# Kernel tuning notes

Measured on AMD Instinct MI355X. Metric: run time of the kernel, lower is better.

Reference implementation:

```python
import jax, jax.numpy as jnp
import numpy as np

N_CLUSTERS = 8
N_DIMS = 4
N_POINTS = 2_000_000


def setup_inputs() -> dict:
    key = jax.random.key(0)
    k1, k2, k3, k4 = jax.random.split(key, 4)
    return {
        "X": jax.random.normal(k1, (N_POINTS, N_DIMS), dtype=jnp.float32),
        "means": jax.random.normal(k2, (N_CLUSTERS, N_DIMS), dtype=jnp.float32),
        "chols": jax.random.normal(k3, (N_CLUSTERS, N_DIMS, N_DIMS), dtype=jnp.float32),
        "weights": jax.random.normal(k4, (N_CLUSTERS,), dtype=jnp.float32),
        "it": 0,
    }


def reference(X, means, chols, weights, it):
    N, D = X.shape
    K = means.shape[0]
    # sigmas[k] = tril(L_k) @ tril(L_k)^T + I  (cholesky_comp)
    L = jnp.tril(chols)                                   # [K,D,D]
    sigmas = L @ jnp.swapaxes(L, -1, -2) + jnp.eye(D, dtype=X.dtype)
    S_inv = jnp.linalg.inv(sigmas)                        # [K,D,D]
    dets = jnp.linalg.det(sigmas)                         # [K]
    two_pi_D = (2.0 * jnp.pi) ** D
    # per-cluster Gaussian densities over all points: dens[k,n]
    diff = X[None, :, :] - means[:, None, :]              # [K,N,D]
    mahal = jnp.einsum('knd,kde,kne->kn', diff, S_inv, diff)  # [K,N]
    dens = jnp.exp(-0.5 * mahal) / jnp.sqrt(two_pi_D * dets)[:, None]
    # pairwise softmax weights over all K^2 (i,j) products w_i*w_j
    wij = weights[:, None] * weights[None, :]             # [K,K]
    W = jax.nn.softmax(wij.reshape(-1)).reshape(K, K)
    # squared-mixture normaliser: z = sum_ij W_ij * N(mu_i; mu_j, S_i+S_j)
    Ssum = sigmas[:, None] + sigmas[None, :]              # [K,K,D,D]
    det_sum = jnp.linalg.det(Ssum)                        # [K,K]
    mdiff = means[:, None, :] - means[None, :, :]         # [K,K,D]
    md = jnp.einsum('ijd,ijde,ije->ij', mdiff, jnp.linalg.inv(Ssum), mdiff)
    norm_term = jnp.exp(-0.5 * md) / jnp.sqrt(two_pi_D * det_sum)
    z = jnp.sum(W * norm_term)
    # numerator: sum_ij W_ij dens_i dens_j  (factored to avoid [K^2,N])
    num = jnp.einsum('in,jn,ij->n', dens, dens, W)        # [N]
    pdf = num / z
    # forward: -(logsumexp over points of log pdf) / N
    out = -(jax.scipy.special.logsumexp(jnp.log(pdf)) / N)
    return out
```

## Files before the change

kernel.cpp:

```cpp
#include <hip/hip_runtime.h>
#include <math.h>


#define KC 8

struct WsLayout {
  double P[36];
  double W[64];
  double logz;
  double pad_;
  float a2[8][10];
  float bb[8][4];
  float cc[8];
};

__device__ inline void chol4(const double S[4][4], double G[4][4]) {
  #pragma unroll
  for (int i = 0; i < 4; ++i) {
    #pragma unroll
    for (int j = 0; j < 4; ++j) {
      if (j > i) { G[i][j] = 0.0; continue; }
      double s = S[i][j];
      #pragma unroll
      for (int m = 0; m < 4; ++m) if (m < j) s -= G[i][m] * G[j][m];
      if (i == j) G[i][j] = sqrt(s);
      else        G[i][j] = s / G[j][j];
    }
  }
}

__global__ void prep_kernel(const float* __restrict__ means,
                            const float* __restrict__ chols,
                            const float* __restrict__ weights,
                            WsLayout* ws) {
  __shared__ double sig[8][4][4];
  const double LOG2E = 1.4426950408889634074;
  const double LN2PI = 1.8378770664093454836;
  const int t = threadIdx.x;

  if (t < 8) {
    const int k = t;
    double L[4][4], S[4][4];
    #pragma unroll
    for (int i = 0; i < 4; ++i)
      #pragma unroll
      for (int j = 0; j < 4; ++j)
        L[i][j] = (j <= i) ? (double)chols[k * 16 + i * 4 + j] : 0.0;
    #pragma unroll
    for (int i = 0; i < 4; ++i)
      #pragma unroll
      for (int j = 0; j < 4; ++j) {
        double s = (i == j) ? 1.0 : 0.0;
        #pragma unroll
        for (int m = 0; m < 4; ++m) s += L[i][m] * L[j][m];
        S[i][j] = s;
        sig[k][i][j] = s;
      }
    double G[4][4];
    chol4(S, G);
    const double logdet =
        2.0 * (log(G[0][0]) + log(G[1][1]) + log(G[2][2]) + log(G[3][3]));
    double Gi[4][4];
    #pragma unroll
    for (int j = 0; j < 4; ++j) {
      #pragma unroll
      for (int i = 0; i < 4; ++i) {
        if (i < j) { Gi[i][j] = 0.0; continue; }
        double s = (i == j) ? 1.0 : 0.0;
        #pragma unroll
        for (int m = 0; m < 4; ++m)
          if (m >= j && m < i) s -= G[i][m] * Gi[m][j];
        Gi[i][j] = s / G[i][i];
      }
    }
    double A[4][4];
    #pragma unroll
    for (int i = 0; i < 4; ++i)
      #pragma unroll
      for (int j = 0; j < 4; ++j) {
        double s = 0.0;
        #pragma unroll
        for (int m = 0; m < 4; ++m) s += Gi[m][i] * Gi[m][j];
        A[i][j] = s;
      }
    double mu[4];
    #pragma unroll
    for (int i = 0; i < 4; ++i) mu[i] = (double)means[k * 4 + i];
    double bmu[4];
    #pragma unroll
    for (int i = 0; i < 4; ++i) {
      double s = 0.0;
      #pragma unroll
      for (int j = 0; j < 4; ++j) s += A[i][j] * mu[j];
      bmu[i] = s;
    }
    double muAmu = 0.0;
    #pragma unroll
    for (int i = 0; i < 4; ++i) muAmu += mu[i] * bmu[i];
    const double logcoef = -0.5 * (4.0 * LN2PI + logdet);
    int tt = 0;
    #pragma unroll
    for (int i = 0; i < 4; ++i)
      #pragma unroll
      for (int j = i; j < 4; ++j, ++tt)
        ws->a2[k][tt] =
            (float)(-0.5 * LOG2E * A[i][j] * ((i == j) ? 1.0 : 2.0));
    #pragma unroll
    for (int i = 0; i < 4; ++i) ws->bb[k][i] = (float)(LOG2E * bmu[i]);
    ws->cc[k] = (float)(LOG2E * (logcoef - 0.5 * muAmu));
  }
  __syncthreads();

  const int i = t >> 3, j = t & 7;
  const double wij = (double)weights[i] * (double)weights[j];
  double m = wij;
  #pragma unroll
  for (int o = 32; o > 0; o >>= 1) {
    double x = __shfl_xor(m, o, 64);
    m = fmax(m, x);
  }
  const double e = exp(wij - m);
  double ssum = e;
  #pragma unroll
  for (int o = 32; o > 0; o >>= 1) ssum += __shfl_xor(ssum, o, 64);
  const double Wij = e / ssum;

  double SS[4][4];
  #pragma unroll
  for (int a = 0; a < 4; ++a)
    #pragma unroll
    for (int b = 0; b < 4; ++b) SS[a][b] = sig[i][a][b] + sig[j][a][b];
  double G2[4][4];
  chol4(SS, G2);
  const double logdetS =
      2.0 * (log(G2[0][0]) + log(G2[1][1]) + log(G2[2][2]) + log(G2[3][3]));
  double bvec[4], y[4];
  #pragma unroll
  for (int a = 0; a < 4; ++a)
    bvec[a] = (double)means[i * 4 + a] - (double)means[j * 4 + a];
  #pragma unroll
  for (int a = 0; a < 4; ++a) {
    double s = bvec[a];
    #pragma unroll
    for (int mm = 0; mm < 4; ++mm) if (mm < a) s -= G2[a][mm] * y[mm];
    y[a] = s / G2[a][a];
  }
  const double md = y[0]*y[0] + y[1]*y[1] + y[2]*y[2] + y[3]*y[3];
  double zterm = Wij * exp(-0.5 * md - 0.5 * (4.0 * LN2PI + logdetS));
  #pragma unroll
  for (int o = 32; o > 0; o >>= 1) zterm += __shfl_xor(zterm, o, 64);
  if (t == 0) ws->logz = log(zterm);
  ws->W[t] = Wij;
  if (t < 36) ws->P[t] = 0.0;
}

__global__ __launch_bounds__(256) void point_kernel(
    const float4* __restrict__ X, const float* __restrict__ par,
    double* __restrict__ accg, int n) {
  float a2[8][10], bb[8][4], cc[8];
  #pragma unroll
  for (int k = 0; k < 8; ++k) {
    #pragma unroll
    for (int u = 0; u < 10; ++u) a2[k][u] = par[k * 10 + u];
    #pragma unroll
    for (int u = 0; u < 4; ++u) bb[k][u] = par[80 + k * 4 + u];
    cc[k] = par[112 + k];
  }
  float acc[36];
  #pragma unroll
  for (int u = 0; u < 36; ++u) acc[u] = 0.0f;

  const int idx = blockIdx.x * blockDim.x + threadIdx.x;
  const int stride = gridDim.x * blockDim.x;
  for (int i = idx; i < n; i += stride) {
    const float4 v = X[i];
    const float p[10] = {v.x * v.x, v.x * v.y, v.x * v.z, v.x * v.w,
                         v.y * v.y, v.y * v.z, v.y * v.w,
                         v.z * v.z, v.z * v.w, v.w * v.w};
    float d[8];
    #pragma unroll
    for (int k = 0; k < 8; ++k) {
      float a = cc[k];
      #pragma unroll
      for (int u = 0; u < 10; ++u) a = fmaf(a2[k][u], p[u], a);
      a = fmaf(bb[k][0], v.x, a);
      a = fmaf(bb[k][1], v.y, a);
      a = fmaf(bb[k][2], v.z, a);
      a = fmaf(bb[k][3], v.w, a);
      d[k] = __builtin_amdgcn_exp2f(a);
    }
    int u = 0;
    #pragma unroll
    for (int a_ = 0; a_ < 8; ++a_)
      #pragma unroll
      for (int b_ = a_; b_ < 8; ++b_, ++u)
        acc[u] = fmaf(d[a_], d[b_], acc[u]);
  }

  const int lane = threadIdx.x & 63;
  const int wid = threadIdx.x >> 6;
  __shared__ float lred[4][36];
  #pragma unroll
  for (int u = 0; u < 36; ++u) {
    float vv = acc[u];
    #pragma unroll
    for (int o = 32; o > 0; o >>= 1) vv += __shfl_xor(vv, o, 64);
    if (lane == 0) lred[wid][u] = vv;
  }
  __syncthreads();
  if (threadIdx.x < 36) {
    const double s = (double)lred[0][threadIdx.x] + (double)lred[1][threadIdx.x] +
                     (double)lred[2][threadIdx.x] + (double)lred[3][threadIdx.x];
    unsafeAtomicAdd(&accg[threadIdx.x], s);
  }
}

__global__ void final_kernel(const WsLayout* __restrict__ ws,
                             float* __restrict__ out, int n) {
  double tot = 0.0;
  int u = 0;
  #pragma unroll
  for (int i = 0; i < 8; ++i)
    #pragma unroll
    for (int j = i; j < 8; ++j, ++u) {
      const double w = ws->W[i * 8 + j] * ((i == j) ? 1.0 : 2.0);
      tot += w * ws->P[u];
    }
  out[0] = (float)(-(log(tot) - ws->logz) / (double)n);
}

extern "C" void kernel_launch(void* const* d_in, const int* in_sizes, int n_in,
                              void* d_out, int out_size, void* d_ws, size_t ws_size,
                              hipStream_t stream) {
  const float* X       = (const float*)d_in[0];
  const float* means   = (const float*)d_in[1];
  const float* chols   = (const float*)d_in[2];
  const float* weights = (const float*)d_in[3];
  const int npoints = in_sizes[0] / 4;

  WsLayout* ws = (WsLayout*)d_ws;
  prep_kernel<<<1, 64, 0, stream>>>(means, chols, weights, ws);
  point_kernel<<<1024, 256, 0, stream>>>((const float4*)X, &ws->a2[0][0],
                                         ws->P, npoints);
  final_kernel<<<1, 1, 0, stream>>>(ws, (float*)d_out, npoints);
}
```

Before: 117.2 us.

## Spread atomics over 32 slots, batch 4 loads per thread, double grid

Global atomic accumulation now goes to 32 separate copies of each of the 36 sums, indexed by block, which are reduced in a 64-thread final kernel. The point loop loads 4 points per iteration to raise memory-level parallelism, using a large negative bias to zero out points past the end. The grid doubles to 2048 blocks and launch bounds request 4 blocks per SM. These changes target atomic contention and load latency, at the cost of more register pressure and a larger workspace zeroed by the prep kernel.

```diff
diff --git a/kernel.cpp b/kernel.cpp
--- a/kernel.cpp
+++ b/kernel.cpp
@@ -2,13 +2,10 @@
 #include <math.h>
 
 
-#define KC 8
-
 struct WsLayout {
-  double P[36];
-  double W[64];
+  double P[36][32];
+  double Wp[36];
   double logz;
-  double pad_;
   float a2[8][10];
   float bb[8][4];
   float cc[8];
@@ -150,11 +147,16 @@
   #pragma unroll
   for (int o = 32; o > 0; o >>= 1) zterm += __shfl_xor(zterm, o, 64);
   if (t == 0) ws->logz = log(zterm);
-  ws->W[t] = Wij;
-  if (t < 36) ws->P[t] = 0.0;
-}
-
-__global__ __launch_bounds__(256) void point_kernel(
+
+  if (i <= j) {
+    const int u = 8 * i - (i * (i - 1)) / 2 + (j - i);
+    ws->Wp[u] = Wij * ((i == j) ? 1.0 : 2.0);
+  }
+  double* Pf = &ws->P[0][0];
+  for (int u = t; u < 36 * 32; u += 64) Pf[u] = 0.0;
+}
+
+__global__ __launch_bounds__(256, 4) void point_kernel(
     const float4* __restrict__ X, const float* __restrict__ par,
     double* __restrict__ accg, int n) {
   float a2[8][10], bb[8][4], cc[8];
@@ -170,31 +172,43 @@
   #pragma unroll
   for (int u = 0; u < 36; ++u) acc[u] = 0.0f;
 
+  const int S = gridDim.x * blockDim.x;
   const int idx = blockIdx.x * blockDim.x + threadIdx.x;
-  const int stride = gridDim.x * blockDim.x;
-  for (int i = idx; i < n; i += stride) {
-    const float4 v = X[i];
-    const float p[10] = {v.x * v.x, v.x * v.y, v.x * v.z, v.x * v.w,
-                         v.y * v.y, v.y * v.z, v.y * v.w,
-                         v.z * v.z, v.z * v.w, v.w * v.w};
-    float d[8];
-    #pragma unroll
-    for (int k = 0; k < 8; ++k) {
-      float a = cc[k];
-      #pragma unroll
-      for (int u = 0; u < 10; ++u) a = fmaf(a2[k][u], p[u], a);
-      a = fmaf(bb[k][0], v.x, a);
-      a = fmaf(bb[k][1], v.y, a);
-      a = fmaf(bb[k][2], v.z, a);
-      a = fmaf(bb[k][3], v.w, a);
-      d[k] = __builtin_amdgcn_exp2f(a);
-    }
-    int u = 0;
-    #pragma unroll
-    for (int a_ = 0; a_ < 8; ++a_)
-      #pragma unroll
-      for (int b_ = a_; b_ < 8; ++b_, ++u)
-        acc[u] = fmaf(d[a_], d[b_], acc[u]);
+  for (int base = idx; base < n; base += 4 * S) {
+    float4 v[4];
+    float kill[4];
+    #pragma unroll
+    for (int j = 0; j < 4; ++j) {
+      const int ij = base + j * S;
+      const bool ok = ij < n;
+      kill[j] = ok ? 0.0f : -1.0e30f;
+      v[j] = X[ok ? ij : 0];
+    }
+    #pragma unroll
+    for (int j = 0; j < 4; ++j) {
+      const float4 vv = v[j];
+      const float p[10] = {vv.x * vv.x, vv.x * vv.y, vv.x * vv.z, vv.x * vv.w,
+                           vv.y * vv.y, vv.y * vv.z, vv.y * vv.w,
+                           vv.z * vv.z, vv.z * vv.w, vv.w * vv.w};
+      float d[8];
+      #pragma unroll
+      for (int k = 0; k < 8; ++k) {
+        float a = cc[k] + kill[j];
+        #pragma unroll
+        for (int u = 0; u < 10; ++u) a = fmaf(a2[k][u], p[u], a);
+        a = fmaf(bb[k][0], vv.x, a);
+        a = fmaf(bb[k][1], vv.y, a);
+        a = fmaf(bb[k][2], vv.z, a);
+        a = fmaf(bb[k][3], vv.w, a);
+        d[k] = __builtin_amdgcn_exp2f(a);
+      }
+      int u = 0;
+      #pragma unroll
+      for (int a_ = 0; a_ < 8; ++a_)
+        #pragma unroll
+        for (int b_ = a_; b_ < 8; ++b_, ++u)
+          acc[u] = fmaf(d[a_], d[b_], acc[u]);
+    }
   }
 
   const int lane = threadIdx.x & 63;
@@ -211,22 +225,23 @@
   if (threadIdx.x < 36) {
     const double s = (double)lred[0][threadIdx.x] + (double)lred[1][threadIdx.x] +
                      (double)lred[2][threadIdx.x] + (double)lred[3][threadIdx.x];
-    unsafeAtomicAdd(&accg[threadIdx.x], s);
+    unsafeAtomicAdd(&accg[threadIdx.x * 32 + (blockIdx.x & 31)], s);
   }
 }
 
 __global__ void final_kernel(const WsLayout* __restrict__ ws,
                              float* __restrict__ out, int n) {
-  double tot = 0.0;
-  int u = 0;
-  #pragma unroll
-  for (int i = 0; i < 8; ++i)
-    #pragma unroll
-    for (int j = i; j < 8; ++j, ++u) {
-      const double w = ws->W[i * 8 + j] * ((i == j) ? 1.0 : 2.0);
-      tot += w * ws->P[u];
-    }
-  out[0] = (float)(-(log(tot) - ws->logz) / (double)n);
+  const int t = threadIdx.x;
+  double val = 0.0;
+  if (t < 36) {
+    double s = 0.0;
+    #pragma unroll
+    for (int b = 0; b < 32; ++b) s += ws->P[t][b];
+    val = ws->Wp[t] * s;
+  }
+  #pragma unroll
+  for (int o = 32; o > 0; o >>= 1) val += __shfl_xor(val, o, 64);
+  if (t == 0) out[0] = (float)(-(log(val) - ws->logz) / (double)n);
 }
 
 extern "C" void kernel_launch(void* const* d_in, const int* in_sizes, int n_in,
@@ -240,7 +255,7 @@
 
   WsLayout* ws = (WsLayout*)d_ws;
   prep_kernel<<<1, 64, 0, stream>>>(means, chols, weights, ws);
-  point_kernel<<<1024, 256, 0, stream>>>((const float4*)X, &ws->a2[0][0],
-                                         ws->P, npoints);
-  final_kernel<<<1, 1, 0, stream>>>(ws, (float*)d_out, npoints);
-}
+  point_kernel<<<2048, 256, 0, stream>>>((const float4*)X, &ws->a2[0][0],
+                                         &ws->P[0][0], npoints);
+  final_kernel<<<1, 64, 0, stream>>>(ws, (float*)d_out, npoints);
+}
```

Result: faster. 112.2 us (-4.3%).
